# Kernel tuning notes

Measured on AMD Instinct MI355X. Metric: run time of the kernel, lower is better.

Reference implementation:

```python
import jax, jax.numpy as jnp
import numpy as np

V = 20000          # number of nodes
E = 100000         # number of edges
NODE_IN = 128      # node_in_feats
EDGE_IN = 128      # edge_in_feats
H = 64             # node_hidden_feats (== GRU hidden, == NNConv in/out)
EDGE_HID = 128     # edge_hidden_feats
OUT = 64           # node_out_feats
STEPS = 9          # num_step_message_passing


def _lin(key, out_f, in_f):
    kw, kb = jax.random.split(key)
    s = 1.0 / np.sqrt(in_f)
    w = jax.random.uniform(kw, (out_f, in_f), jnp.float32, -s, s)
    b = jax.random.uniform(kb, (out_f,), jnp.float32, -s, s)
    return w, b


def setup_inputs() -> dict:
    key = jax.random.key(0)
    ks = jax.random.split(key, 16)
    node_feats = jax.random.normal(ks[0], (V, NODE_IN), jnp.float32)
    edge_feats = jax.random.normal(ks[1], (E, EDGE_IN), jnp.float32)
    src = jax.random.randint(ks[2], (E,), 0, V, jnp.int32)
    dst = jax.random.randint(ks[3], (E,), 0, V, jnp.int32)

    w_p1, b_p1 = _lin(ks[4], H, NODE_IN)          # project_node_feats[0]
    w_p2, b_p2 = _lin(ks[5], H, H)                # project_node_feats[2]
    w_e1, b_e1 = _lin(ks[6], EDGE_HID, EDGE_IN)   # edge_network[0]
    w_e2, b_e2 = _lin(ks[7], H * H, EDGE_HID)     # edge_network[2]
    b_conv = jnp.zeros((H,), jnp.float32)         # NNConv bias
    # GRU: gates stacked [r, z, n] (PyTorch order)
    sg = 1.0 / np.sqrt(H)
    w_ih = jax.random.uniform(ks[8], (3 * H, H), jnp.float32, -sg, sg)
    w_hh = jax.random.uniform(ks[9], (3 * H, H), jnp.float32, -sg, sg)
    b_ih = jax.random.uniform(ks[10], (3 * H,), jnp.float32, -sg, sg)
    b_hh = jax.random.uniform(ks[11], (3 * H,), jnp.float32, -sg, sg)
    w_d1, b_d1 = _lin(ks[12], H, H)               # decoder[0]
    w_d2, b_d2 = _lin(ks[13], OUT, H)             # decoder[2]

    return {
        "node_feats": node_feats, "edge_feats": edge_feats,
        "src": src, "dst": dst,
        "w_p1": w_p1, "b_p1": b_p1, "w_p2": w_p2, "b_p2": b_p2,
        "w_e1": w_e1, "b_e1": b_e1, "w_e2": w_e2, "b_e2": b_e2,
        "b_conv": b_conv,
        "w_ih": w_ih, "w_hh": w_hh, "b_ih": b_ih, "b_hh": b_hh,
        "w_d1": w_d1, "b_d1": b_d1, "w_d2": w_d2, "b_d2": b_d2,
    }


def _mpnn(node_feats, edge_feats, src, dst,
          w_p1, b_p1, w_p2, b_p2, w_e1, b_e1, w_e2, b_e2, b_conv,
          w_ih, w_hh, b_ih, b_hh, w_d1, b_d1, w_d2, b_d2):
    n_nodes = node_feats.shape[0]
    # project_node_feats: Linear -> ReLU -> Linear
    h = jax.nn.relu(node_feats @ w_p1.T + b_p1) @ w_p2.T + b_p2   # (V, H)
    hidden = h
    # edge_network is a pure function of static edge_feats: compute once.
    We = jax.nn.relu(edge_feats @ w_e1.T + b_e1) @ w_e2.T + b_e2  # (E, H*H)
    We = We.reshape(-1, H, H)                                     # (E, in, out)

    def step(carry, _):
        h, hidden = carry
        # NNConv: gather src feats, per-edge matmul, scatter-sum to dst
        msg = jnp.einsum('ei,eio->eo', h[src], We)                # (E, H)
        agg = jax.ops.segment_sum(msg, dst, num_segments=n_nodes) + b_conv
        x = jax.nn.relu(agg)                                      # (V, H)
        # GRUCell (PyTorch gate order r, z, n)
        gi = x @ w_ih.T + b_ih
        gh = hidden @ w_hh.T + b_hh
        i_r, i_z, i_n = jnp.split(gi, 3, axis=-1)
        h_r, h_z, h_n = jnp.split(gh, 3, axis=-1)
        r = jax.nn.sigmoid(i_r + h_r)
        z = jax.nn.sigmoid(i_z + h_z)
        n = jnp.tanh(i_n + r * h_n)
        new_h = (1.0 - z) * n + z * hidden
        return (new_h, new_h), None

    (h, hidden), _ = jax.lax.scan(step, (h, hidden), None, length=STEPS)
    # decoder: Linear -> ReLU -> Linear
    return jax.nn.relu(h @ w_d1.T + b_d1) @ w_d2.T + b_d2


def reference(node_feats, edge_feats, src, dst,
              w_p1, b_p1, w_p2, b_p2, w_e1, b_e1, w_e2, b_e2, b_conv,
              w_ih, w_hh, b_ih, b_hh, w_d1, b_d1, w_d2, b_d2):
    return _mpnn(node_feats, edge_feats, src, dst,
                 w_p1, b_p1, w_p2, b_p2, w_e1, b_e1, w_e2, b_e2, b_conv,
                 w_ih, w_hh, b_ih, b_hh, w_d1, b_d1, w_d2, b_d2)
```

## Files before the change

kernel.cpp:

```cpp
#include <hip/hip_runtime.h>

#define V_N 20000
#define E_N 100000
#define NODE_IN_F 128
#define EDGE_IN_F 128
#define H 64
#define EDGE_HID 128
#define OUT_F 64
#define STEPS 9

typedef __attribute__((ext_vector_type(8))) short bf16x8;
typedef __attribute__((ext_vector_type(4))) float f32x4;

__device__ __forceinline__ unsigned short f2bf(float f) {
    union { float f; unsigned int u; } v; v.f = f;
    unsigned int u = v.u;
    unsigned int r = (u + 0x7fffu + ((u >> 16) & 1u)) >> 16;
    return (unsigned short)r;
}

__device__ __forceinline__ float dot4(float4 w, float4 x) {
    return w.x * x.x + w.y * x.y + w.z * x.z + w.w * x.w;
}

__global__ __launch_bounds__(64) void k_project(
    const float* __restrict__ nf,
    const float* __restrict__ w1, const float* __restrict__ b1,
    const float* __restrict__ w2, const float* __restrict__ b2,
    const float* __restrict__ b2e,
    float* __restrict__ h, float* __restrict__ agg, float* __restrict__ hb)
{
    int v = blockIdx.x, t = threadIdx.x;
    __shared__ float x[NODE_IN_F], tm[H];
    const float* row = nf + (size_t)v * NODE_IN_F;
    x[t] = row[t];
    x[t + 64] = row[t + 64];
    agg[(size_t)v * H + t] = 0.f;
    __syncthreads();
    float acc = b1[t];
    const float4* wr = (const float4*)(w1 + (size_t)t * NODE_IN_F);
    #pragma unroll
    for (int q = 0; q < NODE_IN_F / 4; ++q) acc += dot4(wr[q], *(const float4*)&x[q * 4]);
    tm[t] = fmaxf(acc, 0.f);
    __syncthreads();
    float acc2 = b2[t];
    const float4* wr2 = (const float4*)(w2 + (size_t)t * H);
    #pragma unroll
    for (int q = 0; q < H / 4; ++q) acc2 += dot4(wr2[q], *(const float4*)&tm[q * 4]);
    h[(size_t)v * H + t] = acc2;
    __syncthreads();
    x[t] = acc2;
    __syncthreads();
    float acc3 = 0.f;
    for (int i = 0; i < H; ++i) acc3 += x[i] * b2e[i * 64 + t];
    hb[(size_t)v * H + t] = acc3;
}

__global__ __launch_bounds__(256) void k_edge_g(
    const float* __restrict__ ef,
    const float* __restrict__ w1, const float* __restrict__ b1,
    unsigned short* __restrict__ g)
{
    int tid = threadIdx.x;
    int e0 = blockIdx.x * 32;
    int c = tid & 127, eg = tid >> 7;
    __shared__ float xe[32][132];
    for (int idx = tid; idx < 1024; idx += 256) {
        int e = idx >> 5, kq = idx & 31;
        float4 v = *(const float4*)(ef + (size_t)(e0 + e) * EDGE_IN_F + kq * 4);
        *(float4*)&xe[e][kq * 4] = v;
    }
    __syncthreads();
    float acc[16];
    #pragma unroll
    for (int j = 0; j < 16; ++j) acc[j] = b1[c];
    const float4* wr = (const float4*)(w1 + (size_t)c * EDGE_IN_F);
    for (int kb = 0; kb < EDGE_IN_F / 4; ++kb) {
        float4 w = wr[kb];
        #pragma unroll
        for (int j = 0; j < 16; ++j) {
            float4 x = *(const float4*)&xe[eg * 16 + j][kb * 4];
            acc[j] += dot4(w, x);
        }
    }
    #pragma unroll
    for (int j = 0; j < 16; ++j)
        g[(size_t)(e0 + eg * 16 + j) * EDGE_HID + c] = f2bf(fmaxf(acc[j], 0.f));
}

__global__ __launch_bounds__(256) void k_w2bf(
    const float* __restrict__ w2, unsigned short* __restrict__ w2b)
{
    int idx = blockIdx.x * 256 + threadIdx.x;
    float4 v = *(const float4*)(w2 + (size_t)idx * 4);
    ushort4 o;
    o.x = f2bf(v.x); o.y = f2bf(v.y); o.z = f2bf(v.z); o.w = f2bf(v.w);
    *(ushort4*)(w2b + (size_t)idx * 4) = o;
}

__global__ __launch_bounds__(256) void k_msg_fused(
    const float* __restrict__ h, const unsigned short* __restrict__ g,
    const unsigned short* __restrict__ w2b, const float* __restrict__ hb,
    const int* __restrict__ src, const int* __restrict__ dst,
    float* __restrict__ agg)
{
    int tid = threadIdx.x;
    int wv = tid >> 6, lane = tid & 63;
    int m = lane & 15, q = lane >> 4;
    int e0 = blockIdx.x * 64;
    int o0 = wv * 16;
    __shared__ float h_t[64][68];
    __shared__ int src_s[64], dst_s[64];
    if (tid < 64) {
        int ee = e0 + tid; if (ee > E_N - 1) ee = E_N - 1;
        src_s[tid] = src[ee]; dst_s[tid] = dst[ee];
    }
    __syncthreads();
    for (int idx = tid; idx < 64 * 64; idx += 256) {
        int e = idx >> 6, i = idx & 63;
        h_t[i][e] = h[(size_t)src_s[e] * H + i];
    }
    bf16x8 a[4][4];
    #pragma unroll
    for (int eg = 0; eg < 4; ++eg) {
        int er = e0 + eg * 16 + m; if (er > E_N - 1) er = E_N - 1;
        const unsigned short* ga = g + (size_t)er * EDGE_HID + q * 8;
        #pragma unroll
        for (int kb = 0; kb < 4; ++kb) a[eg][kb] = *(const bf16x8*)(ga + kb * 32);
    }
    __syncthreads();
    f32x4 msg[4] = {{0.f,0.f,0.f,0.f},{0.f,0.f,0.f,0.f},{0.f,0.f,0.f,0.f},{0.f,0.f,0.f,0.f}};
    const unsigned short* pb = w2b + (size_t)(o0 + m) * EDGE_HID + q * 8;

#define LOADB(B, I) { \
    const unsigned short* pn = pb + (size_t)((I) & 63) * 8192; \
    _Pragma("unroll") \
    for (int kb = 0; kb < 4; ++kb) B[kb] = *(const bf16x8*)(pn + kb * 32); }

#define COMPUTE(I, B) { \
    _Pragma("unroll") \
    for (int eg = 0; eg < 4; ++eg) { \
        f32x4 d = {0.f, 0.f, 0.f, 0.f}; \
        d = __builtin_amdgcn_mfma_f32_16x16x32_bf16(a[eg][0], B[0], d, 0, 0, 0); \
        d = __builtin_amdgcn_mfma_f32_16x16x32_bf16(a[eg][1], B[1], d, 0, 0, 0); \
        d = __builtin_amdgcn_mfma_f32_16x16x32_bf16(a[eg][2], B[2], d, 0, 0, 0); \
        d = __builtin_amdgcn_mfma_f32_16x16x32_bf16(a[eg][3], B[3], d, 0, 0, 0); \
        float4 hv = *(const float4*)&h_t[(I)][eg * 16 + q * 4]; \
        msg[eg][0] += hv.x * d[0]; \
        msg[eg][1] += hv.y * d[1]; \
        msg[eg][2] += hv.z * d[2]; \
        msg[eg][3] += hv.w * d[3]; } }

    bf16x8 bA[4], bB[4], bC[4], bD[4];
    LOADB(bA, 0) LOADB(bB, 1) LOADB(bC, 2) LOADB(bD, 3)
    for (int ii = 0; ii < 64; ii += 4) {
        COMPUTE(ii + 0, bA) LOADB(bA, ii + 4)
        COMPUTE(ii + 1, bB) LOADB(bB, ii + 5)
        COMPUTE(ii + 2, bC) LOADB(bC, ii + 6)
        COMPUTE(ii + 3, bD) LOADB(bD, ii + 7)
    }
#undef LOADB
#undef COMPUTE

    int o = o0 + m;
    #pragma unroll
    for (int eg = 0; eg < 4; ++eg) {
        #pragma unroll
        for (int r = 0; r < 4; ++r) {
            int el = eg * 16 + q * 4 + r;
            if (e0 + el < E_N) {
                float v = msg[eg][r] + hb[(size_t)src_s[el] * H + o];
                atomicAdd(&agg[(size_t)dst_s[el] * H + o], v);
            }
        }
    }
}

__global__ __launch_bounds__(256) void k_gru(
    float* __restrict__ agg, const float* __restrict__ b_conv,
    const float* __restrict__ w_ih, const float* __restrict__ w_hh,
    const float* __restrict__ b_ih, const float* __restrict__ b_hh,
    const float* __restrict__ b2e,
    float* __restrict__ h, float* __restrict__ hb)
{
    int tid = threadIdx.x;
    int o = tid & 63, grp = tid >> 6;
    int vbase = blockIdx.x * 16;
    __shared__ float xl[16][68], hl[16][68];
    for (int idx = tid; idx < 16 * 64; idx += 256) {
        int n = idx >> 6, i = idx & 63;
        size_t p = (size_t)(vbase + n) * H + i;
        float a = agg[p];
        agg[p] = 0.f;
        xl[n][i] = fmaxf(a + b_conv[i], 0.f);
        hl[n][i] = h[p];
    }
    __syncthreads();
    float gir[4], giz[4], gin[4], ghr[4], ghz[4], ghn[4];
    #pragma unroll
    for (int n = 0; n < 4; ++n) {
        gir[n] = b_ih[o];       ghr[n] = b_hh[o];
        giz[n] = b_ih[64 + o];  ghz[n] = b_hh[64 + o];
        gin[n] = b_ih[128 + o]; ghn[n] = b_hh[128 + o];
    }
    const float4* wir = (const float4*)(w_ih + (size_t)o * H);
    const float4* wiz = (const float4*)(w_ih + (size_t)(64 + o) * H);
    const float4* win = (const float4*)(w_ih + (size_t)(128 + o) * H);
    const float4* whr = (const float4*)(w_hh + (size_t)o * H);
    const float4* whz = (const float4*)(w_hh + (size_t)(64 + o) * H);
    const float4* whn = (const float4*)(w_hh + (size_t)(128 + o) * H);
    #pragma unroll 4
    for (int qq = 0; qq < H / 4; ++qq) {
        float4 a1 = wir[qq], a2 = wiz[qq], a3 = win[qq];
        float4 c1 = whr[qq], c2 = whz[qq], c3 = whn[qq];
        #pragma unroll
        for (int n = 0; n < 4; ++n) {
            float4 xv = *(const float4*)&xl[grp * 4 + n][qq * 4];
            float4 hv = *(const float4*)&hl[grp * 4 + n][qq * 4];
            gir[n] += dot4(a1, xv); giz[n] += dot4(a2, xv); gin[n] += dot4(a3, xv);
            ghr[n] += dot4(c1, hv); ghz[n] += dot4(c2, hv); ghn[n] += dot4(c3, hv);
        }
    }
    float newh[4];
    #pragma unroll
    for (int n = 0; n < 4; ++n) {
        float hv = hl[grp * 4 + n][o];
        float r = 1.f / (1.f + __expf(-(gir[n] + ghr[n])));
        float z = 1.f / (1.f + __expf(-(giz[n] + ghz[n])));
        float na = gin[n] + r * ghn[n];
        float tn = 1.f - 2.f / (__expf(2.f * na) + 1.f);
        newh[n] = (1.f - z) * tn + z * hv;
        h[(size_t)(vbase + grp * 4 + n) * H + o] = newh[n];
    }
    __syncthreads();
    #pragma unroll
    for (int n = 0; n < 4; ++n) xl[grp * 4 + n][o] = newh[n];
    __syncthreads();
    float hbacc[4] = {0.f, 0.f, 0.f, 0.f};
    for (int i = 0; i < H; ++i) {
        float w = b2e[i * 64 + o];
        #pragma unroll
        for (int n = 0; n < 4; ++n) hbacc[n] += xl[grp * 4 + n][i] * w;
    }
    #pragma unroll
    for (int n = 0; n < 4; ++n)
        hb[(size_t)(vbase + grp * 4 + n) * H + o] = hbacc[n];
}

__global__ __launch_bounds__(64) void k_decoder(
    const float* __restrict__ h,
    const float* __restrict__ w1, const float* __restrict__ b1,
    const float* __restrict__ w2, const float* __restrict__ b2,
    float* __restrict__ out)
{
    int v = blockIdx.x, t = threadIdx.x;
    __shared__ float hl[H], tl[H];
    hl[t] = h[(size_t)v * H + t];
    __syncthreads();
    float acc = b1[t];
    const float4* wr = (const float4*)(w1 + (size_t)t * H);
    #pragma unroll
    for (int q = 0; q < H / 4; ++q) acc += dot4(wr[q], *(const float4*)&hl[q * 4]);
    tl[t] = fmaxf(acc, 0.f);
    __syncthreads();
    float acc2 = b2[t];
    const float4* wr2 = (const float4*)(w2 + (size_t)t * H);
    #pragma unroll
    for (int q = 0; q < H / 4; ++q) acc2 += dot4(wr2[q], *(const float4*)&tl[q * 4]);
    out[(size_t)v * OUT_F + t] = acc2;
}

extern "C" void kernel_launch(void* const* d_in, const int* in_sizes, int n_in,
                              void* d_out, int out_size, void* d_ws, size_t ws_size,
                              hipStream_t stream) {
    const float* nf     = (const float*)d_in[0];
    const float* ef     = (const float*)d_in[1];
    const int* src      = (const int*)d_in[2];
    const int* dst      = (const int*)d_in[3];
    const float* w_p1   = (const float*)d_in[4];
    const float* b_p1   = (const float*)d_in[5];
    const float* w_p2   = (const float*)d_in[6];
    const float* b_p2   = (const float*)d_in[7];
    const float* w_e1   = (const float*)d_in[8];
    const float* b_e1   = (const float*)d_in[9];
    const float* w_e2   = (const float*)d_in[10];
    const float* b_e2   = (const float*)d_in[11];
    const float* b_conv = (const float*)d_in[12];
    const float* w_ih   = (const float*)d_in[13];
    const float* w_hh   = (const float*)d_in[14];
    const float* b_ih   = (const float*)d_in[15];
    const float* b_hh   = (const float*)d_in[16];
    const float* w_d1   = (const float*)d_in[17];
    const float* b_d1   = (const float*)d_in[18];
    const float* w_d2   = (const float*)d_in[19];
    const float* b_d2   = (const float*)d_in[20];

    char* ws = (char*)d_ws;
    unsigned short* g   = (unsigned short*)(ws);
    unsigned short* w2b = (unsigned short*)(ws + 25600000LL);
    float* h            = (float*)(ws + 26648576LL);
    float* agg          = (float*)(ws + 31768576LL);
    float* hb           = (float*)(ws + 36888576LL);

    k_project<<<V_N, 64, 0, stream>>>(nf, w_p1, b_p1, w_p2, b_p2, b_e2, h, agg, hb);
    k_edge_g<<<E_N / 32, 256, 0, stream>>>(ef, w_e1, b_e1, g);
    k_w2bf<<<512, 256, 0, stream>>>(w_e2, w2b);
    for (int s = 0; s < STEPS; ++s) {
        k_msg_fused<<<(E_N + 63) / 64, 256, 0, stream>>>(h, g, w2b, hb, src, dst, agg);
        k_gru<<<V_N / 16, 256, 0, stream>>>(agg, b_conv, w_ih, w_hh, b_ih, b_hh, b_e2, h, hb);
    }
    k_decoder<<<V_N, 64, 0, stream>>>(h, w_d1, b_d1, w_d2, b_d2, (float*)d_out);
}
```

Baseline: 3.062 ms.

## Split edge-message K reduction into outer chunks to cut register pressure

The per-edge message kernel now loops over the four 32-wide K chunks on the outside. For each chunk it loads only that chunk's A fragments, streams eight single-chunk B fragments through a deeper prefetch ring, and folds each partial MFMA result into the h-weighted accumulator. This shrinks the live A and B register footprint, which could raise occupancy and hide the latency of the weight loads. In exchange it re-reads the h_t tile from LDS and repeats the scalar FMA accumulation once per chunk. Because the h weighting is linear, the result is unchanged apart from floating-point rounding order.

```diff
diff --git a/kernel.cpp b/kernel.cpp
--- a/kernel.cpp
+++ b/kernel.cpp
@@ -120,47 +120,60 @@
         int e = idx >> 6, i = idx & 63;
         h_t[i][e] = h[(size_t)src_s[e] * H + i];
     }
-    bf16x8 a[4][4];
+    const unsigned short* ga[4];
     #pragma unroll
     for (int eg = 0; eg < 4; ++eg) {
         int er = e0 + eg * 16 + m; if (er > E_N - 1) er = E_N - 1;
-        const unsigned short* ga = g + (size_t)er * EDGE_HID + q * 8;
-        #pragma unroll
-        for (int kb = 0; kb < 4; ++kb) a[eg][kb] = *(const bf16x8*)(ga + kb * 32);
+        ga[eg] = g + (size_t)er * EDGE_HID + q * 8;
     }
     __syncthreads();
     f32x4 msg[4] = {{0.f,0.f,0.f,0.f},{0.f,0.f,0.f,0.f},{0.f,0.f,0.f,0.f},{0.f,0.f,0.f,0.f}};
     const unsigned short* pb = w2b + (size_t)(o0 + m) * EDGE_HID + q * 8;
 
-#define LOADB(B, I) { \
-    const unsigned short* pn = pb + (size_t)((I) & 63) * 8192; \
-    _Pragma("unroll") \
-    for (int kb = 0; kb < 4; ++kb) B[kb] = *(const bf16x8*)(pn + kb * 32); }
-
+    for (int kb = 0; kb < 4; ++kb) {
+        bf16x8 a0 = *(const bf16x8*)(ga[0] + kb * 32);
+        bf16x8 a1 = *(const bf16x8*)(ga[1] + kb * 32);
+        bf16x8 a2 = *(const bf16x8*)(ga[2] + kb * 32);
+        bf16x8 a3 = *(const bf16x8*)(ga[3] + kb * 32);
+        const unsigned short* pbk = pb + kb * 32;
+
+#define LOADB(B, I) { B = *(const bf16x8*)(pbk + (size_t)((I) & 63) * 8192); }
 #define COMPUTE(I, B) { \
-    _Pragma("unroll") \
-    for (int eg = 0; eg < 4; ++eg) { \
-        f32x4 d = {0.f, 0.f, 0.f, 0.f}; \
-        d = __builtin_amdgcn_mfma_f32_16x16x32_bf16(a[eg][0], B[0], d, 0, 0, 0); \
-        d = __builtin_amdgcn_mfma_f32_16x16x32_bf16(a[eg][1], B[1], d, 0, 0, 0); \
-        d = __builtin_amdgcn_mfma_f32_16x16x32_bf16(a[eg][2], B[2], d, 0, 0, 0); \
-        d = __builtin_amdgcn_mfma_f32_16x16x32_bf16(a[eg][3], B[3], d, 0, 0, 0); \
-        float4 hv = *(const float4*)&h_t[(I)][eg * 16 + q * 4]; \
-        msg[eg][0] += hv.x * d[0]; \
-        msg[eg][1] += hv.y * d[1]; \
-        msg[eg][2] += hv.z * d[2]; \
-        msg[eg][3] += hv.w * d[3]; } }
-
-    bf16x8 bA[4], bB[4], bC[4], bD[4];
-    LOADB(bA, 0) LOADB(bB, 1) LOADB(bC, 2) LOADB(bD, 3)
-    for (int ii = 0; ii < 64; ii += 4) {
-        COMPUTE(ii + 0, bA) LOADB(bA, ii + 4)
-        COMPUTE(ii + 1, bB) LOADB(bB, ii + 5)
-        COMPUTE(ii + 2, bC) LOADB(bC, ii + 6)
-        COMPUTE(ii + 3, bD) LOADB(bD, ii + 7)
-    }
+    f32x4 d0 = {0.f,0.f,0.f,0.f}, d1 = {0.f,0.f,0.f,0.f}; \
+    f32x4 d2 = {0.f,0.f,0.f,0.f}, d3 = {0.f,0.f,0.f,0.f}; \
+    d0 = __builtin_amdgcn_mfma_f32_16x16x32_bf16(a0, B, d0, 0, 0, 0); \
+    d1 = __builtin_amdgcn_mfma_f32_16x16x32_bf16(a1, B, d1, 0, 0, 0); \
+    d2 = __builtin_amdgcn_mfma_f32_16x16x32_bf16(a2, B, d2, 0, 0, 0); \
+    d3 = __builtin_amdgcn_mfma_f32_16x16x32_bf16(a3, B, d3, 0, 0, 0); \
+    float4 h0 = *(const float4*)&h_t[(I)][q * 4]; \
+    float4 h1 = *(const float4*)&h_t[(I)][16 + q * 4]; \
+    float4 h2 = *(const float4*)&h_t[(I)][32 + q * 4]; \
+    float4 h3 = *(const float4*)&h_t[(I)][48 + q * 4]; \
+    msg[0][0] += h0.x * d0[0]; msg[0][1] += h0.y * d0[1]; \
+    msg[0][2] += h0.z * d0[2]; msg[0][3] += h0.w * d0[3]; \
+    msg[1][0] += h1.x * d1[0]; msg[1][1] += h1.y * d1[1]; \
+    msg[1][2] += h1.z * d1[2]; msg[1][3] += h1.w * d1[3]; \
+    msg[2][0] += h2.x * d2[0]; msg[2][1] += h2.y * d2[1]; \
+    msg[2][2] += h2.z * d2[2]; msg[2][3] += h2.w * d2[3]; \
+    msg[3][0] += h3.x * d3[0]; msg[3][1] += h3.y * d3[1]; \
+    msg[3][2] += h3.z * d3[2]; msg[3][3] += h3.w * d3[3]; }
+
+        bf16x8 b0, b1v, b2v, b3, b4, b5, b6, b7;
+        LOADB(b0, 0) LOADB(b1v, 1) LOADB(b2v, 2) LOADB(b3, 3)
+        LOADB(b4, 4) LOADB(b5, 5) LOADB(b6, 6) LOADB(b7, 7)
+        for (int ii = 0; ii < 64; ii += 8) {
+            COMPUTE(ii + 0, b0)  LOADB(b0, ii + 8)
+            COMPUTE(ii + 1, b1v) LOADB(b1v, ii + 9)
+            COMPUTE(ii + 2, b2v) LOADB(b2v, ii + 10)
+            COMPUTE(ii + 3, b3)  LOADB(b3, ii + 11)
+            COMPUTE(ii + 4, b4)  LOADB(b4, ii + 12)
+            COMPUTE(ii + 5, b5)  LOADB(b5, ii + 13)
+            COMPUTE(ii + 6, b6)  LOADB(b6, ii + 14)
+            COMPUTE(ii + 7, b7)  LOADB(b7, ii + 15)
+        }
 #undef LOADB
 #undef COMPUTE
+    }
 
     int o = o0 + m;
     #pragma unroll
```

After: 3.141 ms. 2.6% more time.

## Precompute per-node contracted edge weights and gather messages via CSR-by-source

Applied to the files above, without the earlier changes.

Replaces the per-edge contraction of h[src] with the 64x64x128 edge-network weight by first computing a per-source-node matrix N[v] = h[v]·W2 (split hi/lo bf16 for precision) with MFMA, then each edge does a 128-long dot with its hidden edge features. Edges are sorted by source via histogram/scan/scatter so each block loads one node's N matrix into LDS and reuses it across its out-edges. Nodes are processed in four chunks to bound the large N buffer. This trades a much larger intermediate write/read (8192 bf16 per node) and more launches for removing redundant per-edge weight streaming, with extra bf16 rounding of N.

```diff
diff --git a/kernel.cpp b/kernel.cpp
--- a/kernel.cpp
+++ b/kernel.cpp
@@ -8,6 +8,7 @@
 #define EDGE_HID 128
 #define OUT_F 64
 #define STEPS 9
+#define CHUNK 5000
 
 typedef __attribute__((ext_vector_type(8))) short bf16x8;
 typedef __attribute__((ext_vector_type(4))) float f32x4;
@@ -18,7 +19,15 @@
     unsigned int r = (u + 0x7fffu + ((u >> 16) & 1u)) >> 16;
     return (unsigned short)r;
 }
-
+__device__ __forceinline__ float bfbits(unsigned int u16) {
+    union { unsigned int u; float f; } v; v.u = u16 << 16; return v.f;
+}
+__device__ __forceinline__ float dot2bf(unsigned int a, unsigned int b) {
+    union { unsigned int u; float f; } alo, ahi, blo, bhi;
+    alo.u = a << 16; ahi.u = a & 0xffff0000u;
+    blo.u = b << 16; bhi.u = b & 0xffff0000u;
+    return alo.f * blo.f + ahi.f * bhi.f;
+}
 __device__ __forceinline__ float dot4(float4 w, float4 x) {
     return w.x * x.x + w.y * x.y + w.z * x.z + w.w * x.w;
 }
@@ -28,7 +37,9 @@
     const float* __restrict__ w1, const float* __restrict__ b1,
     const float* __restrict__ w2, const float* __restrict__ b2,
     const float* __restrict__ b2e,
-    float* __restrict__ h, float* __restrict__ agg, float* __restrict__ hb)
+    float* __restrict__ h, float* __restrict__ agg, float* __restrict__ hb,
+    unsigned short* __restrict__ hb16, unsigned short* __restrict__ hb16lo,
+    int* __restrict__ deg)
 {
     int v = blockIdx.x, t = threadIdx.x;
     __shared__ float x[NODE_IN_F], tm[H];
@@ -36,6 +47,7 @@
     x[t] = row[t];
     x[t + 64] = row[t + 64];
     agg[(size_t)v * H + t] = 0.f;
+    if (t == 0) deg[v] = 0;
     __syncthreads();
     float acc = b1[t];
     const float4* wr = (const float4*)(w1 + (size_t)t * NODE_IN_F);
@@ -48,6 +60,9 @@
     #pragma unroll
     for (int q = 0; q < H / 4; ++q) acc2 += dot4(wr2[q], *(const float4*)&tm[q * 4]);
     h[(size_t)v * H + t] = acc2;
+    unsigned short hi = f2bf(acc2);
+    hb16[(size_t)v * H + t] = hi;
+    hb16lo[(size_t)v * H + t] = f2bf(acc2 - bfbits(hi));
     __syncthreads();
     x[t] = acc2;
     __syncthreads();
@@ -88,90 +103,129 @@
         g[(size_t)(e0 + eg * 16 + j) * EDGE_HID + c] = f2bf(fmaxf(acc[j], 0.f));
 }
 
-__global__ __launch_bounds__(256) void k_w2bf(
-    const float* __restrict__ w2, unsigned short* __restrict__ w2b)
-{
-    int idx = blockIdx.x * 256 + threadIdx.x;
-    float4 v = *(const float4*)(w2 + (size_t)idx * 4);
-    ushort4 o;
-    o.x = f2bf(v.x); o.y = f2bf(v.y); o.z = f2bf(v.z); o.w = f2bf(v.w);
-    *(ushort4*)(w2b + (size_t)idx * 4) = o;
-}
-
-__global__ __launch_bounds__(256) void k_msg_fused(
-    const float* __restrict__ h, const unsigned short* __restrict__ g,
-    const unsigned short* __restrict__ w2b, const float* __restrict__ hb,
-    const int* __restrict__ src, const int* __restrict__ dst,
-    float* __restrict__ agg)
+__global__ __launch_bounds__(256) void k_w2rr(
+    const float* __restrict__ w2, unsigned short* __restrict__ w2rr)
+{
+    int f = blockIdx.x * 256 + threadIdx.x;
+    int i = f & 63;
+    int c = f >> 6;
+    int o = c >> 7;
+    int k = c & 127;
+    w2rr[f] = f2bf(w2[(size_t)(i * 64 + o) * 128 + k]);
+}
+
+__global__ __launch_bounds__(256) void k_hist(const int* __restrict__ src, int* __restrict__ deg) {
+    int e = blockIdx.x * 256 + threadIdx.x;
+    if (e < E_N) atomicAdd(&deg[src[e]], 1);
+}
+
+__global__ __launch_bounds__(256) void k_scan(
+    const int* __restrict__ deg, int* __restrict__ rowptr, int* __restrict__ cursor)
+{
+    const int CH = 79;
+    int t = threadIdx.x;
+    __shared__ int part[256];
+    int base = t * CH, s = 0;
+    for (int j = 0; j < CH; ++j) { int v = base + j; if (v < V_N) s += deg[v]; }
+    part[t] = s;
+    __syncthreads();
+    if (t == 0) { int run = 0; for (int i = 0; i < 256; ++i) { int x = part[i]; part[i] = run; run += x; } }
+    __syncthreads();
+    int run = part[t];
+    for (int j = 0; j < CH; ++j) {
+        int v = base + j;
+        if (v < V_N) { rowptr[v] = run; cursor[v] = run; run += deg[v]; }
+    }
+    if (t == 255) rowptr[V_N] = E_N;
+}
+
+__global__ __launch_bounds__(256) void k_scatter(
+    const int* __restrict__ src, int* __restrict__ cursor, int* __restrict__ esort)
+{
+    int e = blockIdx.x * 256 + threadIdx.x;
+    if (e < E_N) {
+        int p = atomicAdd(&cursor[src[e]], 1);
+        esort[p] = e;
+    }
+}
+
+__global__ __launch_bounds__(256) void k_nmat(
+    const unsigned short* __restrict__ hb16, const unsigned short* __restrict__ hb16lo,
+    const unsigned short* __restrict__ w2rr,
+    unsigned short* __restrict__ Nc, int vbase)
 {
     int tid = threadIdx.x;
     int wv = tid >> 6, lane = tid & 63;
     int m = lane & 15, q = lane >> 4;
-    int e0 = blockIdx.x * 64;
-    int o0 = wv * 16;
-    __shared__ float h_t[64][68];
-    __shared__ int src_s[64], dst_s[64];
-    if (tid < 64) {
-        int ee = e0 + tid; if (ee > E_N - 1) ee = E_N - 1;
-        src_s[tid] = src[ee]; dst_s[tid] = dst[ee];
-    }
-    __syncthreads();
-    for (int idx = tid; idx < 64 * 64; idx += 256) {
-        int e = idx >> 6, i = idx & 63;
-        h_t[i][e] = h[(size_t)src_s[e] * H + i];
-    }
-    bf16x8 a[4][4];
-    #pragma unroll
-    for (int eg = 0; eg < 4; ++eg) {
-        int er = e0 + eg * 16 + m; if (er > E_N - 1) er = E_N - 1;
-        const unsigned short* ga = g + (size_t)er * EDGE_HID + q * 8;
-        #pragma unroll
-        for (int kb = 0; kb < 4; ++kb) a[eg][kb] = *(const bf16x8*)(ga + kb * 32);
-    }
-    __syncthreads();
-    f32x4 msg[4] = {{0.f,0.f,0.f,0.f},{0.f,0.f,0.f,0.f},{0.f,0.f,0.f,0.f},{0.f,0.f,0.f,0.f}};
-    const unsigned short* pb = w2b + (size_t)(o0 + m) * EDGE_HID + q * 8;
-
-#define LOADB(B, I) { \
-    const unsigned short* pn = pb + (size_t)((I) & 63) * 8192; \
-    _Pragma("unroll") \
-    for (int kb = 0; kb < 4; ++kb) B[kb] = *(const bf16x8*)(pn + kb * 32); }
-
-#define COMPUTE(I, B) { \
-    _Pragma("unroll") \
-    for (int eg = 0; eg < 4; ++eg) { \
-        f32x4 d = {0.f, 0.f, 0.f, 0.f}; \
-        d = __builtin_amdgcn_mfma_f32_16x16x32_bf16(a[eg][0], B[0], d, 0, 0, 0); \
-        d = __builtin_amdgcn_mfma_f32_16x16x32_bf16(a[eg][1], B[1], d, 0, 0, 0); \
-        d = __builtin_amdgcn_mfma_f32_16x16x32_bf16(a[eg][2], B[2], d, 0, 0, 0); \
-        d = __builtin_amdgcn_mfma_f32_16x16x32_bf16(a[eg][3], B[3], d, 0, 0, 0); \
-        float4 hv = *(const float4*)&h_t[(I)][eg * 16 + q * 4]; \
-        msg[eg][0] += hv.x * d[0]; \
-        msg[eg][1] += hv.y * d[1]; \
-        msg[eg][2] += hv.z * d[2]; \
-        msg[eg][3] += hv.w * d[3]; } }
-
-    bf16x8 bA[4], bB[4], bC[4], bD[4];
-    LOADB(bA, 0) LOADB(bB, 1) LOADB(bC, 2) LOADB(bD, 3)
-    for (int ii = 0; ii < 64; ii += 4) {
-        COMPUTE(ii + 0, bA) LOADB(bA, ii + 4)
-        COMPUTE(ii + 1, bB) LOADB(bB, ii + 5)
-        COMPUTE(ii + 2, bC) LOADB(bC, ii + 6)
-        COMPUTE(ii + 3, bD) LOADB(bD, ii + 7)
-    }
-#undef LOADB
-#undef COMPUTE
-
-    int o = o0 + m;
-    #pragma unroll
-    for (int eg = 0; eg < 4; ++eg) {
+    int vl0 = blockIdx.x * 16;
+    int er = vbase + vl0 + m; if (er > V_N - 1) er = V_N - 1;
+    const unsigned short* pa = hb16 + (size_t)er * 64 + q * 8;
+    const unsigned short* pl = hb16lo + (size_t)er * 64 + q * 8;
+    bf16x8 ah0 = *(const bf16x8*)(pa);
+    bf16x8 ah1 = *(const bf16x8*)(pa + 32);
+    bf16x8 al0 = *(const bf16x8*)(pl);
+    bf16x8 al1 = *(const bf16x8*)(pl + 32);
+    #pragma unroll 2
+    for (int t_i = 0; t_i < 32; ++t_i) {
+        int tile = blockIdx.y * 128 + wv * 32 + t_i;
+        int c0 = tile * 16;
+        const unsigned short* pb = w2rr + (size_t)(c0 + m) * 64 + q * 8;
+        bf16x8 b0 = *(const bf16x8*)(pb);
+        bf16x8 b1 = *(const bf16x8*)(pb + 32);
+        f32x4 dacc = {0.f, 0.f, 0.f, 0.f};
+        dacc = __builtin_amdgcn_mfma_f32_16x16x32_bf16(al0, b0, dacc, 0, 0, 0);
+        dacc = __builtin_amdgcn_mfma_f32_16x16x32_bf16(al1, b1, dacc, 0, 0, 0);
+        dacc = __builtin_amdgcn_mfma_f32_16x16x32_bf16(ah0, b0, dacc, 0, 0, 0);
+        dacc = __builtin_amdgcn_mfma_f32_16x16x32_bf16(ah1, b1, dacc, 0, 0, 0);
         #pragma unroll
         for (int r = 0; r < 4; ++r) {
-            int el = eg * 16 + q * 4 + r;
-            if (e0 + el < E_N) {
-                float v = msg[eg][r] + hb[(size_t)src_s[el] * H + o];
-                atomicAdd(&agg[(size_t)dst_s[el] * H + o], v);
+            int vl = vl0 + q * 4 + r;
+            if (vl < CHUNK)
+                Nc[(size_t)vl * 8192 + c0 + m] = f2bf(dacc[r]);
+        }
+    }
+}
+
+__global__ __launch_bounds__(256) void k_msg2(
+    const unsigned short* __restrict__ Nc, const unsigned short* __restrict__ g,
+    const float* __restrict__ hb, const int* __restrict__ rowptr,
+    const int* __restrict__ esort, const int* __restrict__ dst,
+    float* __restrict__ agg, int vbase)
+{
+    int tid = threadIdx.x;
+    int wv = tid >> 6, lane = tid & 63;
+    int v0 = vbase + blockIdx.x * 8;
+    int vend = vbase + CHUNK;
+    __shared__ unsigned short n_lds[8192];
+    for (int s = 0; s < 8; ++s) {
+        int v = v0 + s;
+        if (v >= vend) break;
+        int r0 = rowptr[v];
+        int d = rowptr[v + 1] - r0;
+        if (d == 0) continue;
+        __syncthreads();
+        const uint4* Ng = (const uint4*)(Nc + (size_t)(v - vbase) * 8192);
+        #pragma unroll
+        for (int rr = 0; rr < 4; ++rr) {
+            int rdi = tid + rr * 256;
+            uint4 val = Ng[rdi];
+            int o = rdi >> 4, kc = rdi & 15;
+            *(uint4*)&n_lds[(kc * 64 + o) * 8] = val;
+        }
+        __syncthreads();
+        float hbv = hb[(size_t)v * 64 + lane];
+        for (int j = wv; j < d; j += 4) {
+            int e = esort[r0 + j];
+            const uint4* ge = (const uint4*)(g + (size_t)e * 128);
+            float acc = 0.f;
+            #pragma unroll
+            for (int kc = 0; kc < 16; ++kc) {
+                uint4 gc = ge[kc];
+                uint4 nc = *(const uint4*)&n_lds[(kc * 64 + lane) * 8];
+                acc += dot2bf(gc.x, nc.x) + dot2bf(gc.y, nc.y)
+                     + dot2bf(gc.z, nc.z) + dot2bf(gc.w, nc.w);
             }
+            atomicAdd(&agg[(size_t)dst[e] * 64 + lane], acc + hbv);
         }
     }
 }
@@ -181,7 +235,8 @@
     const float* __restrict__ w_ih, const float* __restrict__ w_hh,
     const float* __restrict__ b_ih, const float* __restrict__ b_hh,
     const float* __restrict__ b2e,
-    float* __restrict__ h, float* __restrict__ hb)
+    float* __restrict__ h, float* __restrict__ hb,
+    unsigned short* __restrict__ hb16, unsigned short* __restrict__ hb16lo)
 {
     int tid = threadIdx.x;
     int o = tid & 63, grp = tid >> 6;
@@ -230,7 +285,11 @@
         float na = gin[n] + r * ghn[n];
         float tn = 1.f - 2.f / (__expf(2.f * na) + 1.f);
         newh[n] = (1.f - z) * tn + z * hv;
-        h[(size_t)(vbase + grp * 4 + n) * H + o] = newh[n];
+        size_t p = (size_t)(vbase + grp * 4 + n) * H + o;
+        h[p] = newh[n];
+        unsigned short hi = f2bf(newh[n]);
+        hb16[p] = hi;
+        hb16lo[p] = f2bf(newh[n] - bfbits(hi));
     }
     __syncthreads();
     #pragma unroll
@@ -296,18 +355,39 @@
     const float* b_d2   = (const float*)d_in[20];
 
     char* ws = (char*)d_ws;
-    unsigned short* g   = (unsigned short*)(ws);
-    unsigned short* w2b = (unsigned short*)(ws + 25600000LL);
-    float* h            = (float*)(ws + 26648576LL);
-    float* agg          = (float*)(ws + 31768576LL);
-    float* hb           = (float*)(ws + 36888576LL);
-
-    k_project<<<V_N, 64, 0, stream>>>(nf, w_p1, b_p1, w_p2, b_p2, b_e2, h, agg, hb);
+    size_t off = 0;
+    unsigned short* g      = (unsigned short*)(ws + off); off += 25600000;
+    unsigned short* w2rr   = (unsigned short*)(ws + off); off += 1048576;
+    float* h               = (float*)(ws + off);          off += 5120000;
+    float* agg             = (float*)(ws + off);          off += 5120000;
+    float* hb              = (float*)(ws + off);          off += 5120000;
+    unsigned short* hb16   = (unsigned short*)(ws + off); off += 2560000;
+    unsigned short* hb16lo = (unsigned short*)(ws + off); off += 2560000;
+    int* deg               = (int*)(ws + off);            off += 80896;
+    int* cursor            = (int*)(ws + off);            off += 80896;
+    int* rowptr            = (int*)(ws + off);            off += 80896;
+    int* esort             = (int*)(ws + off);            off += 400384;
+    unsigned short* Nc     = (unsigned short*)(ws + off); off += 81920000;
+
+    k_project<<<V_N, 64, 0, stream>>>(nf, w_p1, b_p1, w_p2, b_p2, b_e2,
+                                      h, agg, hb, hb16, hb16lo, deg);
     k_edge_g<<<E_N / 32, 256, 0, stream>>>(ef, w_e1, b_e1, g);
-    k_w2bf<<<512, 256, 0, stream>>>(w_e2, w2b);
+    k_w2rr<<<2048, 256, 0, stream>>>(w_e2, w2rr);
+    k_hist<<<(E_N + 255) / 256, 256, 0, stream>>>(src, deg);
+    k_scan<<<1, 256, 0, stream>>>(deg, rowptr, cursor);
+    k_scatter<<<(E_N + 255) / 256, 256, 0, stream>>>(src, cursor, esort);
+
+    const int NT = (CHUNK + 15) / 16;
+    const int NB2 = (CHUNK + 7) / 8;
     for (int s = 0; s < STEPS; ++s) {
-        k_msg_fused<<<(E_N + 63) / 64, 256, 0, stream>>>(h, g, w2b, hb, src, dst, agg);
-        k_gru<<<V_N / 16, 256, 0, stream>>>(agg, b_conv, w_ih, w_hh, b_ih, b_hh, b_e2, h, hb);
+        for (int c = 0; c < 4; ++c) {
+            int vbase = c * CHUNK;
+            dim3 g1(NT, 4);
+            k_nmat<<<g1, 256, 0, stream>>>(hb16, hb16lo, w2rr, Nc, vbase);
+            k_msg2<<<NB2, 256, 0, stream>>>(Nc, g, hb, rowptr, esort, dst, agg, vbase);
+        }
+        k_gru<<<V_N / 16, 256, 0, stream>>>(agg, b_conv, w_ih, w_hh, b_ih, b_hh,
+                                            b_e2, h, hb, hb16, hb16lo);
     }
     k_decoder<<<V_N, 64, 0, stream>>>(h, w_d1, b_d1, w_d2, b_d2, (float*)d_out);
 }
```

After: 4.689 ms. +53.2%, slower.
